# Performance work log

Hardware: AMD Instinct MI355X
Metric: run time of the kernel (lower is better)

Reference implementation:

```python
import jax, jax.numpy as jnp
import numpy as np

WINDOW = 3
FILTER = 6
FEATURE = 768
SEQ = 256
PAD = WINDOW // 2


def setup_inputs() -> dict:
    key = jax.random.key(0)
    k1, k2, k3 = jax.random.split(key, 3)
    B = 256
    inputs = jax.random.normal(k1, (B, SEQ, FEATURE), dtype=jnp.float32)
    # per-position Linear weights: torch nn.Linear stores [out, in]; we keep [S, in, out]
    bound = 1.0 / np.sqrt(WINDOW * FEATURE)
    W = jax.random.uniform(k2, (SEQ, WINDOW * FEATURE, FILTER), dtype=jnp.float32,
                           minval=-bound, maxval=bound)
    b = jax.random.uniform(k3, (SEQ, FILTER), dtype=jnp.float32,
                           minval=-bound, maxval=bound)
    return {"inputs": inputs, "W": W, "b": b}


def reference(inputs, W, b):
    # inputs: [B, S, F]. Pad along sequence with zeros (matches F.pad on transposed tensor).
    padded = jnp.pad(inputs, ((0, 0), (PAD, PAD), (0, 0)))  # [B, S+2p, F]
    # Vectorized sliding-window gather: idx [S, W]
    idx = jnp.arange(SEQ)[:, None] + jnp.arange(WINDOW)[None, :]
    windows = padded[:, idx, :]                              # [B, S, W, F]
    Bsz = windows.shape[0]
    windows = windows.reshape(Bsz, SEQ, WINDOW * FEATURE)    # [B, S, W*F]
    # Per-position distinct Linear + ReLU (Dropout is identity at inference)
    out = jnp.einsum('bsf,sfo->bso', windows, W) + b[None, :, :]
    return jax.nn.relu(out)
```

## Files before the change

kernel.cpp:

```cpp
#include <hip/hip_runtime.h>

#define SEQ     256
#define FEAT    768
#define WIN     3
#define FILT    6
#define KTOT    (WIN * FEAT)
#define WELEMS  (KTOT * FILT)
#define NB      8
#define BLOCK   768
#define NWAVES  12
#define NGROUPS 32
#define RSTR    49

__global__ __launch_bounds__(BLOCK, 3)
void pos_linear_kernel(const float* __restrict__ x,
                       const float* __restrict__ W,
                       const float* __restrict__ bias,
                       float* __restrict__ out) {
    __shared__ float wlds[WELEMS];
    __shared__ float red[2][NWAVES * RSTR];

    const int blk = blockIdx.x;
    const int s   = ((blk & 7) << 5) | (blk >> 3);
    const int tid = threadIdx.x;

    {
        const float4* src = (const float4*)(W + (size_t)s * WELEMS);
        float4*       dst = (float4*)wlds;
        for (int i = tid; i < WELEMS / 4; i += BLOCK) dst[i] = src[i];
    }

    const int lane = tid & 63;
    const int wave = tid >> 6;
    const int w    = wave >> 2;
    const int q    = wave & 3;
    const int r    = s - 1 + w;
    const bool valid = (r >= 0) && (r < SEQ);
    const int  f0   = 192 * q + lane;
    const int  k0   = FEAT * w + f0;
    const float* xrow = valid ? (x + (size_t)r * FEAT + f0) : x;

    const int gidx = ((lane & 1) << 3) | ((lane & 2) << 1) |
                     ((lane & 4) >> 1) | ((lane & 8) >> 3);

    __syncthreads();

    for (int g = 0; g < NGROUPS; ++g) {
        const int b0 = g * NB;

        float v[NB * FILT];
        #pragma unroll
        for (int i = 0; i < NB * FILT; ++i) v[i] = 0.f;

        if (valid) {
            #pragma unroll
            for (int j = 0; j < 3; ++j) {
                const int kj = k0 + 64 * j;
                float wv[FILT];
                #pragma unroll
                for (int o = 0; o < FILT; ++o) wv[o] = wlds[kj * FILT + o];

                float xv[NB];
                #pragma unroll
                for (int nb = 0; nb < NB; ++nb)
                    xv[nb] = xrow[(size_t)(b0 + nb) * (SEQ * FEAT) + 64 * j];

                #pragma unroll
                for (int nb = 0; nb < NB; ++nb)
                    #pragma unroll
                    for (int o = 0; o < FILT; ++o)
                        v[nb * FILT + o] = fmaf(xv[nb], wv[o], v[nb * FILT + o]);
            }
        }

        #pragma unroll
        for (int step = 0; step < 4; ++step) {
            const int m    = 1 << step;
            const int half = 48 >> (step + 1);
            const bool upper = (lane & m) != 0;
            #pragma unroll
            for (int j = 0; j < half; ++j) {
                float snd = upper ? v[j] : v[j + half];
                float kep = upper ? v[j + half] : v[j];
                v[j] = kep + __shfl_xor(snd, m, 64);
            }
        }
        #pragma unroll
        for (int j = 0; j < 3; ++j) {
            v[j] += __shfl_xor(v[j], 16, 64);
            v[j] += __shfl_xor(v[j], 32, 64);
        }

        float* rb = red[g & 1];
        if (lane < 16) {
            #pragma unroll
            for (int j = 0; j < 3; ++j)
                rb[wave * RSTR + 3 * gidx + j] = v[j];
        }
        __syncthreads();

        const int ft = tid - ((g % NWAVES) << 6);
        if (ft >= 0 && ft < 48) {
            float sum = 0.f;
            #pragma unroll
            for (int vw = 0; vw < NWAVES; ++vw) sum += rb[vw * RSTR + ft];
            const int nb = ft / FILT;
            const int o  = ft - nb * FILT;
            float val = sum + bias[s * FILT + o];
            val = val > 0.f ? val : 0.f;
            out[((size_t)(b0 + nb) * SEQ + s) * FILT + o] = val;
        }
    }
}

extern "C" void kernel_launch(void* const* d_in, const int* in_sizes, int n_in,
                              void* d_out, int out_size, void* d_ws, size_t ws_size,
                              hipStream_t stream) {
    const float* x   = (const float*)d_in[0];
    const float* W   = (const float*)d_in[1];
    const float* b   = (const float*)d_in[2];
    float*       out = (float*)d_out;
    (void)in_sizes; (void)n_in; (void)out_size; (void)d_ws; (void)ws_size;
    pos_linear_kernel<<<SEQ, BLOCK, 0, stream>>>(x, W, b, out);
}
```

Measured before the change: 322.7 us.

## Use split-bf16 MFMA for per-position linear with batch-tiled waves

Replaces the scalar FMA plus shuffle/LDS reduction with bf16x3 MFMA (hi*hi + hi*lo + lo*hi) on 16x16x32 tiles. Each wave handles 16 batch rows over the full K=2304, so no cross-wave reduction or per-group syncs are needed. Weights are converted once per block into hi/lo bf16 in LDS, and the grid is doubled to 512 blocks with 512 threads. Only 6 of the 16 MFMA output columns are used, and the split precision trades some accuracy for matrix-core throughput. The kernel is memory bound on reading x (~200MB), so the gain mainly comes from cutting reduction and sync overhead.

New measurement: 336.7 us. 1.04x slower.

```diff
diff --git a/kernel.cpp b/kernel.cpp
--- a/kernel.cpp
+++ b/kernel.cpp
@@ -1,114 +1,107 @@
 #include <hip/hip_runtime.h>
 
-#define SEQ     256
-#define FEAT    768
-#define WIN     3
-#define FILT    6
-#define KTOT    (WIN * FEAT)
-#define WELEMS  (KTOT * FILT)
-#define NB      8
-#define BLOCK   768
-#define NWAVES  12
-#define NGROUPS 32
-#define RSTR    49
+#define SEQ   256
+#define FEAT  768
+#define FILT  6
+#define WELEMS (2304 * FILT)
 
-__global__ __launch_bounds__(BLOCK, 3)
+typedef __attribute__((ext_vector_type(8))) short s16x8;
+typedef __attribute__((ext_vector_type(4))) float f32x4;
+
+__global__ __launch_bounds__(512, 4)
 void pos_linear_kernel(const float* __restrict__ x,
                        const float* __restrict__ W,
                        const float* __restrict__ bias,
                        float* __restrict__ out) {
-    __shared__ float wlds[WELEMS];
-    __shared__ float red[2][NWAVES * RSTR];
+    __shared__ __align__(16) unsigned short wb[2 * 13824];
 
-    const int blk = blockIdx.x;
-    const int s   = ((blk & 7) << 5) | (blk >> 3);
-    const int tid = threadIdx.x;
+    const int blk   = blockIdx.x;
+    const int halfb = blk >> 8;
+    const int sb    = blk & 255;
+    const int s     = ((sb & 7) << 5) | (sb >> 3);
+    const int tid   = threadIdx.x;
 
     {
-        const float4* src = (const float4*)(W + (size_t)s * WELEMS);
-        float4*       dst = (float4*)wlds;
-        for (int i = tid; i < WELEMS / 4; i += BLOCK) dst[i] = src[i];
+        const float* Ws = W + (size_t)s * WELEMS;
+        for (int k = tid; k < 2304; k += 512) {
+            const int slot8 = (k >> 3) * 6;
+            const int e     = k & 7;
+            #pragma unroll
+            for (int o = 0; o < FILT; ++o) {
+                float f = Ws[k * FILT + o];
+                unsigned int bi = __float_as_uint(f);
+                float rem = f - __uint_as_float(bi & 0xffff0000u);
+                wb[(slot8 + o) * 8 + e]         = (unsigned short)(bi >> 16);
+                wb[13824 + (slot8 + o) * 8 + e] =
+                    (unsigned short)(__float_as_uint(rem) >> 16);
+            }
+        }
     }
+    __syncthreads();
 
     const int lane = tid & 63;
     const int wave = tid >> 6;
-    const int w    = wave >> 2;
-    const int q    = wave & 3;
-    const int r    = s - 1 + w;
-    const bool valid = (r >= 0) && (r < SEQ);
-    const int  f0   = 192 * q + lane;
-    const int  k0   = FEAT * w + f0;
-    const float* xrow = valid ? (x + (size_t)r * FEAT + f0) : x;
+    const int row  = lane & 15;
+    const int h    = lane >> 4;
+    const int col  = lane & 15;
+    const bool cv  = col < FILT;
+    const int b0   = (halfb << 7) + (wave << 4);
 
-    const int gidx = ((lane & 1) << 3) | ((lane & 2) << 1) |
-                     ((lane & 4) >> 1) | ((lane & 8) >> 3);
+    const int bidx = (6 * h + col) * 8;
+    const s16x8 z8 = {0, 0, 0, 0, 0, 0, 0, 0};
 
-    __syncthreads();
+    f32x4 acc_hh = {0, 0, 0, 0};
+    f32x4 acc_hl = {0, 0, 0, 0};
+    f32x4 acc_lh = {0, 0, 0, 0};
 
-    for (int g = 0; g < NGROUPS; ++g) {
-        const int b0 = g * NB;
+    const float* xb = x + (size_t)(b0 + row) * (SEQ * FEAT) + 8 * h;
 
-        float v[NB * FILT];
+    auto step = [&](f32x4 u, f32x4 v, int tg) {
+        s16x8 ah, al;
         #pragma unroll
-        for (int i = 0; i < NB * FILT; ++i) v[i] = 0.f;
+        for (int e = 0; e < 8; ++e) {
+            float f = (e < 4) ? u[e] : v[e - 4];
+            unsigned int bi = __float_as_uint(f);
+            ah[e] = (short)(bi >> 16);
+            float rem = f - __uint_as_float(bi & 0xffff0000u);
+            al[e] = (short)(__float_as_uint(rem) >> 16);
+        }
+        s16x8 bh = cv ? *(const s16x8*)&wb[bidx + 192 * tg]         : z8;
+        s16x8 bl = cv ? *(const s16x8*)&wb[13824 + bidx + 192 * tg] : z8;
+        acc_hh = __builtin_amdgcn_mfma_f32_16x16x32_bf16(ah, bh, acc_hh, 0, 0, 0);
+        acc_hl = __builtin_amdgcn_mfma_f32_16x16x32_bf16(ah, bl, acc_hl, 0, 0, 0);
+        acc_lh = __builtin_amdgcn_mfma_f32_16x16x32_bf16(al, bh, acc_lh, 0, 0, 0);
+    };
 
-        if (valid) {
-            #pragma unroll
-            for (int j = 0; j < 3; ++j) {
-                const int kj = k0 + 64 * j;
-                float wv[FILT];
-                #pragma unroll
-                for (int o = 0; o < FILT; ++o) wv[o] = wlds[kj * FILT + o];
+    #pragma unroll
+    for (int w = 0; w < 3; ++w) {
+        const int r = s - 1 + w;
+        if (r < 0 || r >= SEQ) continue;
+        const f32x4* ap = (const f32x4*)(xb + (size_t)r * FEAT);
+        const int tb = 24 * w;
 
-                float xv[NB];
-                #pragma unroll
-                for (int nb = 0; nb < NB; ++nb)
-                    xv[nb] = xrow[(size_t)(b0 + nb) * (SEQ * FEAT) + 64 * j];
+        f32x4 cu = ap[0], cw = ap[1];
+        f32x4 nu = ap[8], nw = ap[9];
+        #pragma unroll 2
+        for (int t = 0; t < 22; ++t) {
+            f32x4 fu = cu, fv = cw;
+            cu = nu; cw = nw;
+            nu = ap[8 * t + 16];
+            nw = ap[8 * t + 17];
+            step(fu, fv, tb + t);
+        }
+        step(cu, cw, tb + 22);
+        step(nu, nw, tb + 23);
+    }
 
-                #pragma unroll
-                for (int nb = 0; nb < NB; ++nb)
-                    #pragma unroll
-                    for (int o = 0; o < FILT; ++o)
-                        v[nb * FILT + o] = fmaf(xv[nb], wv[o], v[nb * FILT + o]);
-            }
-        }
-
+    if (cv) {
+        const float bv = bias[s * FILT + col];
         #pragma unroll
-        for (int step = 0; step < 4; ++step) {
-            const int m    = 1 << step;
-            const int half = 48 >> (step + 1);
-            const bool upper = (lane & m) != 0;
-            #pragma unroll
-            for (int j = 0; j < half; ++j) {
-                float snd = upper ? v[j] : v[j + half];
-                float kep = upper ? v[j + half] : v[j];
-                v[j] = kep + __shfl_xor(snd, m, 64);
-            }
-        }
-        #pragma unroll
-        for (int j = 0; j < 3; ++j) {
-            v[j] += __shfl_xor(v[j], 16, 64);
-            v[j] += __shfl_xor(v[j], 32, 64);
-        }
-
-        float* rb = red[g & 1];
-        if (lane < 16) {
-            #pragma unroll
-            for (int j = 0; j < 3; ++j)
-                rb[wave * RSTR + 3 * gidx + j] = v[j];
-        }
-        __syncthreads();
-
-        const int ft = tid - ((g % NWAVES) << 6);
-        if (ft >= 0 && ft < 48) {
-            float sum = 0.f;
-            #pragma unroll
-            for (int vw = 0; vw < NWAVES; ++vw) sum += rb[vw * RSTR + ft];
-            const int nb = ft / FILT;
-            const int o  = ft - nb * FILT;
-            float val = sum + bias[s * FILT + o];
-            val = val > 0.f ? val : 0.f;
-            out[((size_t)(b0 + nb) * SEQ + s) * FILT + o] = val;
+        for (int g = 0; g < 4; ++g) {
+            const int b = b0 + 4 * h + g;
+            float vsum = acc_hh[g] + acc_hl[g] + acc_lh[g] + bv;
+            vsum = vsum > 0.f ? vsum : 0.f;
+            out[((size_t)b * SEQ + s) * FILT + col] = vsum;
         }
     }
 }
@@ -121,5 +114,5 @@
     const float* b   = (const float*)d_in[2];
     float*       out = (float*)d_out;
     (void)in_sizes; (void)n_in; (void)out_size; (void)d_ws; (void)ws_size;
-    pos_linear_kernel<<<SEQ, BLOCK, 0, stream>>>(x, W, b, out);
+    pos_linear_kernel<<<SEQ * 2, 512, 0, stream>>>(x, W, b, out);
 }
```
